# Kernel optimization log

Hardware: AMD Instinct MI355X
Metric: run time of the kernel (lower is better)

## Reference

```python
import jax, jax.numpy as jnp
import numpy as np

B = 32          # batch_size
S = 64          # num_subgraph
D = 8           # dim_multi_hot (module-level global in source repo)
NE = S * D      # num_edges = 512
NNODES = 1024
E = 150000      # incidence rows
IN_UNITS = [16, 32, 32]
OUT_UNITS = [32, 32, 16]


def _glorot(key, shape):
    # glorot_normal over last two dims (out, in)
    fan_out, fan_in = shape[-2], shape[-1]
    std = (2.0 / (fan_in + fan_out)) ** 0.5
    return std * jax.random.normal(key, shape, dtype=jnp.float32)


def setup_inputs() -> dict:
    key = jax.random.key(0)
    ks = jax.random.split(key, 10)
    nodes_features = jax.random.normal(ks[0], (NNODES * S, IN_UNITS[0]), dtype=jnp.float32)
    c0 = jax.random.randint(ks[1], (E,), 0, B, dtype=jnp.int32)
    c1 = jax.random.randint(ks[2], (E,), 0, NNODES, dtype=jnp.int32)
    c2 = jax.random.randint(ks[3], (E,), 0, S, dtype=jnp.int32)
    c3 = jax.random.randint(ks[4], (E,), 0, D, dtype=jnp.int32)
    incidence_matrix = jnp.stack([c0, c1, c2, c3], axis=1)
    return {
        'nodes_features': nodes_features,
        'in_core0': _glorot(ks[5], (NE, IN_UNITS[1], IN_UNITS[0])),
        'in_bias0': jnp.zeros((NE, IN_UNITS[1], 1), jnp.float32),
        'in_core1': _glorot(ks[6], (NE, IN_UNITS[2], IN_UNITS[1])),
        'in_bias1': jnp.zeros((NE, IN_UNITS[2], 1), jnp.float32),
        'out_core0': _glorot(ks[7], (NE, OUT_UNITS[1], OUT_UNITS[0])),
        'out_bias0': jnp.zeros((NE, OUT_UNITS[1], 1), jnp.float32),
        'out_core1': _glorot(ks[8], (NE, OUT_UNITS[2], OUT_UNITS[1])),
        'out_bias1': jnp.zeros((NE, OUT_UNITS[2], 1), jnp.float32),
        'incidence_matrix': incidence_matrix,
    }


def reference(nodes_features, in_core0, in_bias0, in_core1, in_bias1,
              out_core0, out_bias0, out_core1, out_bias1, incidence_matrix):
    c0 = incidence_matrix[:, 0]
    c1 = incidence_matrix[:, 1]
    c2 = incidence_matrix[:, 2]
    c3 = incidence_matrix[:, 3]

    # gather node features per incidence row: [E, in0]
    x = nodes_features[c1 * S + c2]
    eidx = c2 * D + c3  # per-edge weight index, < NE

    # per-edge MLP (gathered batched matmul + bias + relu)
    for W, b in ((in_core0, in_bias0), (in_core1, in_bias1)):
        x = jax.nn.relu(jnp.einsum('eoi,ei->eo', W[eidx], x) + b[eidx, :, 0])

    # unsorted segment mean over irregular edge groups
    seg = c0 * (D * S) + c2 * D + c3
    nseg = B * S * D
    sums = jax.ops.segment_sum(x, seg, num_segments=nseg)           # [B*NE, 32]
    cnt = jax.ops.segment_sum(jnp.ones((x.shape[0], 1), x.dtype), seg, num_segments=nseg)
    ef = jnp.where(cnt > 0, sums / jnp.maximum(cnt, 1.0), 0.0)       # [B*NE, 32]

    # output MLP: weights tiled over batch (einsum avoids explicit repeat)
    ef = ef.reshape(B, NE, -1)
    for W, b in ((out_core0, out_bias0), (out_core1, out_bias1)):
        ef = jax.nn.relu(jnp.einsum('eoi,bei->beo', W, ef) + b[None, :, :, 0])

    return ef.reshape(B * NE, OUT_UNITS[-1], 1)
```

## Files before the change

kernel.cpp:

```cpp
#include <hip/hip_runtime.h>

#define B_    32
#define S_    64
#define D_    8
#define NE_   512
#define E_    150000
#define CAP   448

#define SC_BLK  1024
#define SC_GRID ((E_ + SC_BLK - 1) / SC_BLK)

typedef __attribute__((ext_vector_type(8)))  short  short8;
typedef __attribute__((ext_vector_type(16))) float  float16;

__device__ __forceinline__ unsigned short f2bf(float f) {
    union { float f; unsigned int u; } cv; cv.f = f;
    unsigned int u = cv.u;
    return (unsigned short)((u + 0x7fffu + ((u >> 16) & 1u)) >> 16);
}
__device__ __forceinline__ unsigned int pack2bf(float a, float b) {
    return (unsigned int)f2bf(a) | ((unsigned int)f2bf(b) << 16);
}

__global__ __launch_bounds__(SC_BLK)
void scatter_csr(const int* __restrict__ inc,
                 int* __restrict__ gcnt,
                 int* __restrict__ payload) {
    __shared__ int lcount[NE_];
    __shared__ int lbase[NE_];
    const int tid = threadIdx.x;

    if (tid < NE_) lcount[tid] = 0;
    __syncthreads();

    const int e = blockIdx.x * SC_BLK + tid;
    int ei = -1, lp = 0, pl = 0;
    if (e < E_) {
        const int4 c = ((const int4*)inc)[e];
        ei = c.z * D_ + c.w;
        pl = (c.x << 16) | (c.y * S_ + c.z);
        lp = atomicAdd(&lcount[ei], 1);
    }
    __syncthreads();

    if (tid < NE_) {
        const int c = lcount[tid];
        lbase[tid] = c ? atomicAdd(&gcnt[tid], c) : 0;
    }
    __syncthreads();

    if (ei >= 0) {
        const int s = lbase[ei] + lp;
        if (s < CAP) payload[ei * CAP + s] = pl;
    }
}


#define TILE_COMPUTE(bXv, pvv, vldv)                                            \
  {                                                                             \
    float16 c0;                                                                 \
    _Pragma("unroll")                                                           \
    for (int r = 0; r < 16; ++r)                                                \
        c0[r] = bias0s[(r & 3) + 8 * (r >> 2) + 4 * q];                         \
    c0 = __builtin_amdgcn_mfma_f32_32x32x16_bf16(aWa, (bXv), c0, 0, 0, 0);      \
    unsigned Pw[8];                                                             \
    _Pragma("unroll")                                                           \
    for (int j = 0; j < 8; ++j)                                                 \
        Pw[j] = pack2bf(fmaxf(c0[2 * j], 0.f), fmaxf(c0[2 * j + 1], 0.f));      \
    asm("v_permlane32_swap_b32 %0, %1" : "+v"(Pw[0]), "+v"(Pw[2]));             \
    asm("v_permlane32_swap_b32 %0, %1" : "+v"(Pw[1]), "+v"(Pw[3]));             \
    asm("v_permlane32_swap_b32 %0, %1" : "+v"(Pw[4]), "+v"(Pw[6]));             \
    asm("v_permlane32_swap_b32 %0, %1" : "+v"(Pw[5]), "+v"(Pw[7]));             \
    union { unsigned u[4]; short8 s; } H0c, H1c;                                \
    H0c.u[0] = Pw[0]; H0c.u[1] = Pw[1]; H0c.u[2] = Pw[2]; H0c.u[3] = Pw[3];     \
    H1c.u[0] = Pw[4]; H1c.u[1] = Pw[5]; H1c.u[2] = Pw[6]; H1c.u[3] = Pw[7];     \
    float16 c1;                                                                 \
    _Pragma("unroll")                                                           \
    for (int r = 0; r < 16; ++r)                                                \
        c1[r] = bias1s[(r & 3) + 8 * (r >> 2) + 4 * q];                         \
    c1 = __builtin_amdgcn_mfma_f32_32x32x16_bf16(aWb0, H0c.s, c1, 0, 0, 0);     \
    c1 = __builtin_amdgcn_mfma_f32_32x32x16_bf16(aWb1, H1c.s, c1, 0, 0, 0);     \
    if (vldv) {                                                                 \
        const int b_e = ((pvv) >> 16) & 31;                                     \
        _Pragma("unroll")                                                       \
        for (int r = 0; r < 16; ++r)                                            \
            atomicAdd(&acc[b_e][(r & 3) + 8 * (r >> 2) + 4 * q],                \
                      fmaxf(c1[r], 0.f));                                       \
        if (q == 0) atomicAdd(&cnts[b_e], 1.f);                                 \
    }                                                                           \
  }

__global__ __launch_bounds__(512, 4)
void main_mfma(const float* __restrict__ nf,
               const float* __restrict__ iw0, const float* __restrict__ ib0,
               const float* __restrict__ iw1, const float* __restrict__ ib1,
               const float* __restrict__ ow0, const float* __restrict__ ob0,
               const float* __restrict__ ow1, const float* __restrict__ ob1,
               const int* __restrict__ gcnt, const int* __restrict__ payload,
               float* __restrict__ out) {
    const int bid  = blockIdx.x;
    const int tid  = threadIdx.x;
    const int lane = tid & 63;
    const int wav  = tid >> 6;
    const int e32  = lane & 31;
    const int q    = lane >> 5;

    __shared__ float acc[32][33];
    __shared__ float hb[32][33];
    __shared__ float cnts[32];
    __shared__ float q0t[32 * 33];
    __shared__ float q1t[32 * 17];
    __shared__ float qb0s[32], qb1s[16];
    __shared__ float bias0s[32], bias1s[32];

    short8 aWa, aWb0, aWb1;
    {
        const float* wa = iw0 + (size_t)bid * 512 + e32 * 16 + q * 8;
        float4 u0 = ((const float4*)wa)[0], u1 = ((const float4*)wa)[1];
        unsigned int p[4] = { pack2bf(u0.x,u0.y), pack2bf(u0.z,u0.w),
                              pack2bf(u1.x,u1.y), pack2bf(u1.z,u1.w) };
        aWa = *(short8*)p;
    }
    {
        const float* wb = iw1 + (size_t)bid * 1024 + e32 * 32 + q * 8;
        float4 u0 = ((const float4*)wb)[0], u1 = ((const float4*)wb)[1];
        unsigned int p[4] = { pack2bf(u0.x,u0.y), pack2bf(u0.z,u0.w),
                              pack2bf(u1.x,u1.y), pack2bf(u1.z,u1.w) };
        aWb0 = *(short8*)p;
        const float* wb2 = wb + 16;
        float4 u2 = ((const float4*)wb2)[0], u3 = ((const float4*)wb2)[1];
        unsigned int p2[4] = { pack2bf(u2.x,u2.y), pack2bf(u2.z,u2.w),
                               pack2bf(u3.x,u3.y), pack2bf(u3.z,u3.w) };
        aWb1 = *(short8*)p2;
    }

    for (int i = tid; i < 1024; i += 512) {
        const int o = i >> 5, k = i & 31;
        q0t[k * 33 + o] = ow0[(size_t)bid * 1024 + i];
    }
    { const int o = tid >> 5, k = tid & 31;
      q1t[k * 17 + o] = ow1[(size_t)bid * 512 + tid]; }
    if (tid < 32)       { bias0s[tid] = ib0[bid * 32 + tid]; cnts[tid] = 0.f; }
    else if (tid < 64)  bias1s[tid - 32] = ib1[bid * 32 + (tid - 32)];
    else if (tid < 96)  qb0s[tid - 64] = ob0[bid * 32 + (tid - 64)];
    else if (tid < 112) qb1s[tid - 96] = ob1[bid * 16 + (tid - 96)];
    for (int i = tid; i < 32 * 33; i += 512) ((float*)acc)[i] = 0.f;

    const int n = min(gcnt[bid], CAP);
    const int ntiles = (n + 31) >> 5;
    const bool h0 = wav < ntiles;
    const bool h1 = (wav + 8) < ntiles;
    int  pv0 = 0, pv1 = 0;
    bool v0 = false, v1 = false;
    short8 bX0 = {}, bX1 = {};
    if (h0) {
        const int s = (wav << 5) + e32;
        v0 = s < n;
        pv0 = payload[bid * CAP + (v0 ? s : n - 1)];
    }
    if (h1) {
        const int s = ((wav + 8) << 5) + e32;
        v1 = s < n;
        pv1 = payload[bid * CAP + (v1 ? s : n - 1)];
    }
    if (h0) {
        const float4* xp = (const float4*)(nf + (size_t)(pv0 & 0xFFFF) * 16 + q * 8);
        float4 u0 = xp[0], u1 = xp[1];
        unsigned int pk[4] = { pack2bf(u0.x,u0.y), pack2bf(u0.z,u0.w),
                               pack2bf(u1.x,u1.y), pack2bf(u1.z,u1.w) };
        bX0 = *(short8*)pk;
    }
    if (h1) {
        const float4* xp = (const float4*)(nf + (size_t)(pv1 & 0xFFFF) * 16 + q * 8);
        float4 u0 = xp[0], u1 = xp[1];
        unsigned int pk[4] = { pack2bf(u0.x,u0.y), pack2bf(u0.z,u0.w),
                               pack2bf(u1.x,u1.y), pack2bf(u1.z,u1.w) };
        bX1 = *(short8*)pk;
    }
    __syncthreads();

    if (h0) TILE_COMPUTE(bX0, pv0, v0);
    if (h1) TILE_COMPUTE(bX1, pv1, v1);
    __syncthreads();

    {
        const int b  = tid >> 4;
        const int j  = tid & 15;
        const float cv  = cnts[b];
        const float inv = cv > 0.f ? 1.0f / cv : 0.0f;
        #pragma unroll
        for (int s = 0; s < 2; ++s) {
            const int oo = j * 2 + s;
            float d = 0.f;
            #pragma unroll
            for (int k = 0; k < 32; ++k) d = fmaf(q0t[k * 33 + oo], acc[b][k], d);
            hb[b][oo] = fmaxf(fmaf(d, inv, qb0s[oo]), 0.f);
        }
    }
    __syncthreads();

    {
        const int b = tid >> 4;
        const int o = tid & 15;
        float d = qb1s[o];
        #pragma unroll
        for (int k = 0; k < 32; ++k) d = fmaf(q1t[k * 17 + o], hb[b][k], d);
        out[((size_t)b * NE_ + bid) * 16 + o] = fmaxf(d, 0.f);
    }
}

extern "C" void kernel_launch(void* const* d_in, const int* in_sizes, int n_in,
                              void* d_out, int out_size, void* d_ws, size_t ws_size,
                              hipStream_t stream) {
    const float* nf  = (const float*)d_in[0];
    const float* iw0 = (const float*)d_in[1];
    const float* ib0 = (const float*)d_in[2];
    const float* iw1 = (const float*)d_in[3];
    const float* ib1 = (const float*)d_in[4];
    const float* ow0 = (const float*)d_in[5];
    const float* ob0 = (const float*)d_in[6];
    const float* ow1 = (const float*)d_in[7];
    const float* ob1 = (const float*)d_in[8];
    const int*   inc = (const int*)d_in[9];

    int* gcnt    = (int*)d_ws;
    int* payload = (int*)((char*)d_ws + 4096);

    hipMemsetAsync(gcnt, 0, NE_ * sizeof(int), stream);
    scatter_csr<<<SC_GRID, SC_BLK, 0, stream>>>(inc, gcnt, payload);
    main_mfma<<<NE_, 512, 0, stream>>>(nf, iw0, ib0, iw1, ib1, ow0, ob0, ow1, ob1,
                                       gcnt, payload, (float*)d_out);
}
```

Before: 120.8 us.

## Fuse CSR scatter into main kernel via cooperative launch and grid syncs

Replaces the memset, scatter kernel and main kernel with a single cooperative kernel of 512 blocks. Each block zeroes its own counter, bins a slice of incidence rows into shared memory, then uses two grid-wide syncs to reserve global slots and write the payload before the per-edge MLP work. This removes two extra launches and the memset, but adds two grid barriers and makes each block stage only about 293 rows, and it depends on all 512 blocks being co-resident.

Result: slower. 242.3 us (+100.6%).

```diff
diff --git a/kernel.cpp b/kernel.cpp
--- a/kernel.cpp
+++ b/kernel.cpp
@@ -1,4 +1,7 @@
 #include <hip/hip_runtime.h>
+#include <hip/hip_cooperative_groups.h>
+
+namespace cg = cooperative_groups;
 
 #define B_    32
 #define S_    64
@@ -6,9 +9,7 @@
 #define NE_   512
 #define E_    150000
 #define CAP   448
-
-#define SC_BLK  1024
-#define SC_GRID ((E_ + SC_BLK - 1) / SC_BLK)
+#define EPB   ((E_ + NE_ - 1) / NE_)
 
 typedef __attribute__((ext_vector_type(8)))  short  short8;
 typedef __attribute__((ext_vector_type(16))) float  float16;
@@ -20,39 +21,6 @@
 }
 __device__ __forceinline__ unsigned int pack2bf(float a, float b) {
     return (unsigned int)f2bf(a) | ((unsigned int)f2bf(b) << 16);
-}
-
-__global__ __launch_bounds__(SC_BLK)
-void scatter_csr(const int* __restrict__ inc,
-                 int* __restrict__ gcnt,
-                 int* __restrict__ payload) {
-    __shared__ int lcount[NE_];
-    __shared__ int lbase[NE_];
-    const int tid = threadIdx.x;
-
-    if (tid < NE_) lcount[tid] = 0;
-    __syncthreads();
-
-    const int e = blockIdx.x * SC_BLK + tid;
-    int ei = -1, lp = 0, pl = 0;
-    if (e < E_) {
-        const int4 c = ((const int4*)inc)[e];
-        ei = c.z * D_ + c.w;
-        pl = (c.x << 16) | (c.y * S_ + c.z);
-        lp = atomicAdd(&lcount[ei], 1);
-    }
-    __syncthreads();
-
-    if (tid < NE_) {
-        const int c = lcount[tid];
-        lbase[tid] = c ? atomicAdd(&gcnt[tid], c) : 0;
-    }
-    __syncthreads();
-
-    if (ei >= 0) {
-        const int s = lbase[ei] + lp;
-        if (s < CAP) payload[ei * CAP + s] = pl;
-    }
 }
 
 
@@ -91,13 +59,14 @@
   }
 
 __global__ __launch_bounds__(512, 4)
-void main_mfma(const float* __restrict__ nf,
-               const float* __restrict__ iw0, const float* __restrict__ ib0,
-               const float* __restrict__ iw1, const float* __restrict__ ib1,
-               const float* __restrict__ ow0, const float* __restrict__ ob0,
-               const float* __restrict__ ow1, const float* __restrict__ ob1,
-               const int* __restrict__ gcnt, const int* __restrict__ payload,
-               float* __restrict__ out) {
+void fused(const float* __restrict__ nf,
+           const float* __restrict__ iw0, const float* __restrict__ ib0,
+           const float* __restrict__ iw1, const float* __restrict__ ib1,
+           const float* __restrict__ ow0, const float* __restrict__ ob0,
+           const float* __restrict__ ow1, const float* __restrict__ ob1,
+           const int* __restrict__ inc,
+           int* __restrict__ gcnt, int* __restrict__ payload,
+           float* __restrict__ out) {
     const int bid  = blockIdx.x;
     const int tid  = threadIdx.x;
     const int lane = tid & 63;
@@ -112,6 +81,12 @@
     __shared__ float q1t[32 * 17];
     __shared__ float qb0s[32], qb1s[16];
     __shared__ float bias0s[32], bias1s[32];
+    __shared__ int   lcount[NE_];
+    __shared__ int   lbase[NE_];
+
+    cg::grid_group grid = cg::this_grid();
+
+    if (tid == 0) gcnt[bid] = 0;
 
     short8 aWa, aWb0, aWb1;
     {
@@ -145,6 +120,33 @@
     else if (tid < 96)  qb0s[tid - 64] = ob0[bid * 32 + (tid - 64)];
     else if (tid < 112) qb1s[tid - 96] = ob1[bid * 16 + (tid - 96)];
     for (int i = tid; i < 32 * 33; i += 512) ((float*)acc)[i] = 0.f;
+
+    if (tid < NE_) lcount[tid] = 0;
+    __syncthreads();
+
+    const int e = bid * EPB + tid;
+    int ei = -1, lp = 0, pl = 0;
+    if (tid < EPB && e < E_) {
+        const int4 c = ((const int4*)inc)[e];
+        ei = c.z * D_ + c.w;
+        pl = (c.x << 16) | (c.y * S_ + c.z);
+        lp = atomicAdd(&lcount[ei], 1);
+    }
+    __syncthreads();
+
+    grid.sync();
+
+    if (tid < NE_) {
+        const int c = lcount[tid];
+        lbase[tid] = c ? atomicAdd(&gcnt[tid], c) : 0;
+    }
+    __syncthreads();
+    if (ei >= 0) {
+        const int s = lbase[ei] + lp;
+        if (s < CAP) payload[ei * CAP + s] = pl;
+    }
+
+    grid.sync();
 
     const int n = min(gcnt[bid], CAP);
     const int ntiles = (n + 31) >> 5;
@@ -177,7 +179,6 @@
                                pack2bf(u1.x,u1.y), pack2bf(u1.z,u1.w) };
         bX1 = *(short8*)pk;
     }
-    __syncthreads();
 
     if (h0) TILE_COMPUTE(bX0, pv0, v0);
     if (h1) TILE_COMPUTE(bX1, pv1, v1);
@@ -223,11 +224,14 @@
     const float* ob1 = (const float*)d_in[8];
     const int*   inc = (const int*)d_in[9];
 
-    int* gcnt    = (int*)d_ws;
-    int* payload = (int*)((char*)d_ws + 4096);
-
-    hipMemsetAsync(gcnt, 0, NE_ * sizeof(int), stream);
-    scatter_csr<<<SC_GRID, SC_BLK, 0, stream>>>(inc, gcnt, payload);
-    main_mfma<<<NE_, 512, 0, stream>>>(nf, iw0, ib0, iw1, ib1, ow0, ob0, ow1, ob1,
-                                       gcnt, payload, (float*)d_out);
-}
+    int*   gcnt    = (int*)d_ws;
+    int*   payload = (int*)((char*)d_ws + 4096);
+    float* outp    = (float*)d_out;
+
+    void* kargs[] = { (void*)&nf,  (void*)&iw0, (void*)&ib0, (void*)&iw1,
+                      (void*)&ib1, (void*)&ow0, (void*)&ob0, (void*)&ow1,
+                      (void*)&ob1, (void*)&inc, (void*)&gcnt, (void*)&payload,
+                      (void*)&outp };
+    hipLaunchCooperativeKernel((const void*)fused, dim3(NE_), dim3(512),
+                               kargs, 0, stream);
+}
```

## Batch scatter elements per thread, pad counters, hoist gathers before weight loads

Applied to the files above, without the earlier changes.

The CSR scatter kernel now handles four incidence rows per thread, so fewer blocks issue global atomics. The per-edge global counters are padded to a 32-int pitch so they no longer share cache lines. The main kernel issues its payload and node-feature gathers first, ahead of the weight loads, and drops the per-tile guards so every wave always computes both tiles with masked validity. The cost is wasted MFMA work on empty tiles and reads of uninitialised payload slots, including past CAP into the next segment or the end of the buffer. It also needs a larger counter memset.

Result: no change. 119.4 us (-1.2%).

```diff
diff --git a/kernel.cpp b/kernel.cpp
--- a/kernel.cpp
+++ b/kernel.cpp
@@ -7,8 +7,12 @@
 #define E_    150000
 #define CAP   448
 
-#define SC_BLK  1024
-#define SC_GRID ((E_ + SC_BLK - 1) / SC_BLK)
+#define SC_BLK   1024
+#define SC_EPT   4
+#define SC_EPB   (SC_BLK * SC_EPT)
+#define SC_GRID  ((E_ + SC_EPB - 1) / SC_EPB)
+
+#define GC_PITCH 32
 
 typedef __attribute__((ext_vector_type(8)))  short  short8;
 typedef __attribute__((ext_vector_type(16))) float  float16;
@@ -33,25 +37,32 @@
     if (tid < NE_) lcount[tid] = 0;
     __syncthreads();
 
-    const int e = blockIdx.x * SC_BLK + tid;
-    int ei = -1, lp = 0, pl = 0;
-    if (e < E_) {
-        const int4 c = ((const int4*)inc)[e];
-        ei = c.z * D_ + c.w;
-        pl = (c.x << 16) | (c.y * S_ + c.z);
-        lp = atomicAdd(&lcount[ei], 1);
+    int ei[SC_EPT], lp[SC_EPT], pl[SC_EPT];
+    #pragma unroll
+    for (int i = 0; i < SC_EPT; ++i) {
+        const int e = blockIdx.x * SC_EPB + i * SC_BLK + tid;
+        ei[i] = -1;
+        if (e < E_) {
+            const int4 c = ((const int4*)inc)[e];
+            ei[i] = c.z * D_ + c.w;
+            pl[i] = (c.x << 16) | (c.y * S_ + c.z);
+            lp[i] = atomicAdd(&lcount[ei[i]], 1);
+        }
     }
     __syncthreads();
 
     if (tid < NE_) {
         const int c = lcount[tid];
-        lbase[tid] = c ? atomicAdd(&gcnt[tid], c) : 0;
-    }
-    __syncthreads();
-
-    if (ei >= 0) {
-        const int s = lbase[ei] + lp;
-        if (s < CAP) payload[ei * CAP + s] = pl;
+        lbase[tid] = c ? atomicAdd(&gcnt[tid * GC_PITCH], c) : 0;
+    }
+    __syncthreads();
+
+    #pragma unroll
+    for (int i = 0; i < SC_EPT; ++i) {
+        if (ei[i] >= 0) {
+            const int s = lbase[ei[i]] + lp[i];
+            if (s < CAP) payload[ei[i] * CAP + s] = pl[i];
+        }
     }
 }
 
@@ -113,6 +124,13 @@
     __shared__ float qb0s[32], qb1s[16];
     __shared__ float bias0s[32], bias1s[32];
 
+    const int n = min(gcnt[bid * GC_PITCH], CAP);
+
+    const int s0 = (wav << 5) + e32;
+    const int s1 = s0 + 256;
+    const int pv0 = payload[bid * CAP + s0];
+    const int pv1 = payload[bid * CAP + s1];
+
     short8 aWa, aWb0, aWb1;
     {
         const float* wa = iw0 + (size_t)bid * 512 + e32 * 16 + q * 8;
@@ -134,6 +152,24 @@
         aWb1 = *(short8*)p2;
     }
 
+    const bool v0 = s0 < n;
+    const bool v1 = s1 < n;
+    short8 bX0, bX1;
+    {
+        const float4* xp = (const float4*)(nf + (size_t)(pv0 & 0xFFFF) * 16 + q * 8);
+        float4 u0 = xp[0], u1 = xp[1];
+        unsigned int pk[4] = { pack2bf(u0.x,u0.y), pack2bf(u0.z,u0.w),
+                               pack2bf(u1.x,u1.y), pack2bf(u1.z,u1.w) };
+        bX0 = *(short8*)pk;
+    }
+    {
+        const float4* xp = (const float4*)(nf + (size_t)(pv1 & 0xFFFF) * 16 + q * 8);
+        float4 u0 = xp[0], u1 = xp[1];
+        unsigned int pk[4] = { pack2bf(u0.x,u0.y), pack2bf(u0.z,u0.w),
+                               pack2bf(u1.x,u1.y), pack2bf(u1.z,u1.w) };
+        bX1 = *(short8*)pk;
+    }
+
     for (int i = tid; i < 1024; i += 512) {
         const int o = i >> 5, k = i & 31;
         q0t[k * 33 + o] = ow0[(size_t)bid * 1024 + i];
@@ -145,42 +181,10 @@
     else if (tid < 96)  qb0s[tid - 64] = ob0[bid * 32 + (tid - 64)];
     else if (tid < 112) qb1s[tid - 96] = ob1[bid * 16 + (tid - 96)];
     for (int i = tid; i < 32 * 33; i += 512) ((float*)acc)[i] = 0.f;
-
-    const int n = min(gcnt[bid], CAP);
-    const int ntiles = (n + 31) >> 5;
-    const bool h0 = wav < ntiles;
-    const bool h1 = (wav + 8) < ntiles;
-    int  pv0 = 0, pv1 = 0;
-    bool v0 = false, v1 = false;
-    short8 bX0 = {}, bX1 = {};
-    if (h0) {
-        const int s = (wav << 5) + e32;
-        v0 = s < n;
-        pv0 = payload[bid * CAP + (v0 ? s : n - 1)];
-    }
-    if (h1) {
-        const int s = ((wav + 8) << 5) + e32;
-        v1 = s < n;
-        pv1 = payload[bid * CAP + (v1 ? s : n - 1)];
-    }
-    if (h0) {
-        const float4* xp = (const float4*)(nf + (size_t)(pv0 & 0xFFFF) * 16 + q * 8);
-        float4 u0 = xp[0], u1 = xp[1];
-        unsigned int pk[4] = { pack2bf(u0.x,u0.y), pack2bf(u0.z,u0.w),
-                               pack2bf(u1.x,u1.y), pack2bf(u1.z,u1.w) };
-        bX0 = *(short8*)pk;
-    }
-    if (h1) {
-        const float4* xp = (const float4*)(nf + (size_t)(pv1 & 0xFFFF) * 16 + q * 8);
-        float4 u0 = xp[0], u1 = xp[1];
-        unsigned int pk[4] = { pack2bf(u0.x,u0.y), pack2bf(u0.z,u0.w),
-                               pack2bf(u1.x,u1.y), pack2bf(u1.z,u1.w) };
-        bX1 = *(short8*)pk;
-    }
-    __syncthreads();
-
-    if (h0) TILE_COMPUTE(bX0, pv0, v0);
-    if (h1) TILE_COMPUTE(bX1, pv1, v1);
+    __syncthreads();
+
+    TILE_COMPUTE(bX0, pv0, v0);
+    TILE_COMPUTE(bX1, pv1, v1);
     __syncthreads();
 
     {
@@ -224,9 +228,9 @@
     const int*   inc = (const int*)d_in[9];
 
     int* gcnt    = (int*)d_ws;
-    int* payload = (int*)((char*)d_ws + 4096);
-
-    hipMemsetAsync(gcnt, 0, NE_ * sizeof(int), stream);
+    int* payload = (int*)((char*)d_ws + NE_ * GC_PITCH * 4);
+
+    hipMemsetAsync(gcnt, 0, NE_ * GC_PITCH * sizeof(int), stream);
     scatter_csr<<<SC_GRID, SC_BLK, 0, stream>>>(inc, gcnt, payload);
     main_mfma<<<NE_, 512, 0, stream>>>(nf, iw0, ib0, iw1, ib1, ow0, ob0, ow1, ob1,
                                        gcnt, payload, (float*)d_out);
```
